# Kernel tuning notes

Measured on AMD Instinct MI355X. Metric: run time of the kernel, lower is better.

The kernel has to match this reference:

```python
import jax, jax.numpy as jnp
import numpy as np

D_MODEL = 1024
NHEAD = 16
HEAD_DIM = D_MODEL // NHEAD
SCALE = 1.0 / np.sqrt(HEAD_DIM).astype(np.float32)
B, L = 2, 2048
NEG_INF = -1e30


def setup_inputs() -> dict:
    key = jax.random.key(0)
    ks = jax.random.split(key, 12)
    xav = np.sqrt(6.0 / (D_MODEL + D_MODEL)).astype(np.float32)  # xavier_uniform gain=1
    def lin_w(k):
        return jax.random.uniform(k, (D_MODEL, D_MODEL), jnp.float32, -xav, xav)
    x = jax.random.normal(ks[0], (B, L, D_MODEL), jnp.float32)
    role_mask = jax.random.randint(ks[1], (B, L), 0, 2, jnp.int32)
    # causal attention mask: True = masked (upper triangle above diagonal)
    attn_mask = jnp.triu(jnp.ones((L, L), jnp.bool_), k=1)
    # random key padding: True = padded key
    key_padding_mask = jax.random.randint(ks[2], (B, L), 0, 2, jnp.int32).astype(jnp.bool_)
    return {
        "x": x,
        "role_mask": role_mask,
        "attn_mask": attn_mask,
        "key_padding_mask": key_padding_mask,
        "Wq": lin_w(ks[3]), "bq": jnp.zeros((D_MODEL,), jnp.float32),
        "Wk": lin_w(ks[4]), "bk": jnp.zeros((D_MODEL,), jnp.float32),
        "Wv": lin_w(ks[5]), "bv": jnp.zeros((D_MODEL,), jnp.float32),
        "Wo": lin_w(ks[6]), "bo": jnp.zeros((D_MODEL,), jnp.float32),
        "delta": jnp.asarray(1.0, jnp.float32),
    }


def reference(x, role_mask, attn_mask, key_padding_mask,
              Wq, bq, Wk, bk, Wv, bv, Wo, bo, delta):
    Bb, Ll, Dd = x.shape
    def heads(t):  # [B,L,D] -> [B,H,L,hd]
        return t.reshape(Bb, Ll, NHEAD, HEAD_DIM).transpose(0, 2, 1, 3)
    Q = heads(x @ Wq.T + bq)
    K = heads(x @ Wk.T + bk)
    V = heads(x @ Wv.T + bv)
    scores = jnp.einsum('bhqd,bhkd->bhqk', Q, K) * SCALE  # [B,H,L,L]
    same_role = (role_mask[:, :, None] == role_mask[:, None, :])  # [B,L,L]
    scores = scores + (same_role.astype(scores.dtype) * delta)[:, None, :, :]
    scores = jnp.where(attn_mask[None, None, :, :], -jnp.inf, scores)
    scores = jnp.where(key_padding_mask[:, None, None, :], -jnp.inf, scores)
    attn = jax.nn.softmax(scores, axis=-1)
    attn = jnp.nan_to_num(attn, nan=0.0, posinf=0.0, neginf=0.0)
    out = jnp.einsum('bhqk,bhkd->bhqd', attn, V)
    out = out.transpose(0, 2, 1, 3).reshape(Bb, Ll, Dd)
    return out @ Wo.T + bo
```

## Files before the change

### kernel.cpp

```cpp
#include <hip/hip_runtime.h>
#include <hip/hip_bf16.h>

#define DM 1024
#define NH 16
#define HD 64
#define BB 2
#define LL 2048
#define SCALE 0.125f
#define NEG_BIG -1e30f
#define LOG2E 1.4426950408889634f
#define SC2 (SCALE * LOG2E)
#define FIXM 16.0f
#define SLOTB 8448
#define POOL0_SLOTS 960

typedef __bf16 bf16;
typedef __bf16 bf16x8 __attribute__((ext_vector_type(8)));
typedef __bf16 bf16x4 __attribute__((ext_vector_type(4)));
typedef float f32x4 __attribute__((ext_vector_type(4)));

static __device__ inline bf16x8 load8(const bf16* p) {
    return *reinterpret_cast<const bf16x8*>(p);
}

static __device__ inline float scrub(float x) {
    union { float f; unsigned u; } c; c.f = x;
    return ((c.u & 0x7F800000u) == 0x7F800000u) ? 0.f : x;
}

typedef __attribute__((address_space(1))) const unsigned char ga_t;
typedef __attribute__((address_space(3))) unsigned char ls_t;
static __device__ inline void gload_lds16(const void* g, void* l) {
    __builtin_amdgcn_global_load_lds((ga_t*)g, (ls_t*)l, 16, 0, 0);
}

__global__ __launch_bounds__(256) void prep_all(
    const float* __restrict__ x,
    const float* __restrict__ Wq, const float* __restrict__ Wk,
    const float* __restrict__ Wv, const float* __restrict__ Wo,
    bf16* __restrict__ xb, bf16* __restrict__ Wqb, bf16* __restrict__ Wkb,
    bf16* __restrict__ Wvb, bf16* __restrict__ Wob,
    const int* __restrict__ role, const void* __restrict__ kpad,
    const float* __restrict__ deltap, float2* __restrict__ biasG)
{
    const int tid = threadIdx.x;
    const int gid = blockIdx.x;
    if (gid < 2048) {
        const float* src; bf16* dst; size_t base;
        if (gid < 1024) { src = x; dst = xb; base = (size_t)gid * 1024; }
        else {
            const int wsel = (gid - 1024) >> 8;
            src = (wsel == 0) ? Wq : (wsel == 1) ? Wk : (wsel == 2) ? Wv : Wo;
            dst = (wsel == 0) ? Wqb : (wsel == 1) ? Wkb : (wsel == 2) ? Wvb : Wob;
            base = (size_t)((gid - 1024) & 255) * 1024;
        }
#pragma unroll
        for (int it = 0; it < 4; it++) {
            const size_t i = base + it * 256 + tid;
            const f32x4 v = ((const f32x4*)src)[i];
            bf16x4 o;
            o[0] = (bf16)v[0]; o[1] = (bf16)v[1]; o[2] = (bf16)v[2]; o[3] = (bf16)v[3];
            ((bf16x4*)dst)[i] = o;
        }
        return;
    }
    const unsigned char* kb = (const unsigned char*)kpad;
    int f3F = 0, fLow = 0, fOff = 0;
    for (int i = (tid & 63); i < BB * LL; i += 64) {
        const unsigned char v = kb[i];
        if (v == 0x3F) f3F = 1;
        if ((i & 3) < 2 && v) fLow = 1;
        if ((i & 3) && v) fOff = 1;
    }
    const int mode = __any(f3F) ? (__any(fLow) ? 3 : 2) : (__any(fOff) ? 1 : 0);
    const float d2 = scrub(deltap[0]) * LOG2E;
    const int idx = (gid - 2048) * 256 + tid;
    const bool pad = (mode == 0) ? (((const int*)kpad)[idx] != 0)
                   : (mode == 1) ? (((const unsigned char*)kpad)[idx] != 0)
                   : (mode == 2) ? (((const float*)kpad)[idx] != 0.f)
                                 : (((const unsigned short*)kpad)[idx] != 0);
    const int r = role[idx];
    const float base = (pad ? NEG_BIG : 0.f) - FIXM;
    float2 o;
    o.x = base + ((r == 0) ? d2 : 0.f);
    o.y = base + ((r == 1) ? d2 : 0.f);
    biasG[idx] = o;
}

__global__ __launch_bounds__(256) void qkv_bf16(
    const bf16* __restrict__ xb,
    const bf16* __restrict__ Wqb, const bf16* __restrict__ Wkb, const bf16* __restrict__ Wvb,
    const float* __restrict__ bq, const float* __restrict__ bk, const float* __restrict__ bv,
    bf16* __restrict__ qw, bf16* __restrict__ kw, bf16* __restrict__ vw)
{
    __shared__ bf16 As[128 * 32];
    __shared__ bf16 Bs[128 * 32];
    const int tid = threadIdx.x;
    const int lane = tid & 63, w = tid >> 6;
    const int wm = w >> 1, wn = w & 1;
    const int ln = lane & 15, quad = lane >> 4;

    const int lin = blockIdx.y * 32 + blockIdx.x;
    const int xcd = lin & 7;
    const int t = lin >> 3;
    const int mloc = t & 3;
    const int yy = t >> 2;
    const int m0 = (xcd * 4 + mloc) * 128;
    const int sel = yy >> 3;
    const int nloc0 = (yy & 7) * 128;

    const bf16* Wb = (sel == 0) ? Wqb : ((sel == 1) ? Wkb : Wvb);
    const float* bias = (sel == 0) ? bq : ((sel == 1) ? bk : bv);
    bf16* dstw = (sel == 0) ? qw : ((sel == 1) ? kw : vw);

    const int rA = lane >> 2;
    const int cA = (lane & 3) * 8;

    f32x4 acc[4][4] = {};
    for (int k0 = 0; k0 < DM; k0 += 32) {
        __syncthreads();
#pragma unroll
        for (int s = 0; s < 2; s++) {
            const int r0 = s * 64 + w * 16;
            gload_lds16(xb + (size_t)(m0 + r0 + rA) * DM + k0 + cA, &As[r0 * 32]);
            gload_lds16(Wb + (size_t)(nloc0 + r0 + rA) * DM + k0 + cA, &Bs[r0 * 32]);
        }
        __syncthreads();
        bf16x8 a[4], b[4];
#pragma unroll
        for (int mi = 0; mi < 4; mi++)
            a[mi] = *(bf16x8*)&As[(wm * 64 + mi * 16 + ln) * 32 + quad * 8];
#pragma unroll
        for (int ni = 0; ni < 4; ni++)
            b[ni] = *(bf16x8*)&Bs[(wn * 64 + ni * 16 + ln) * 32 + quad * 8];
#pragma unroll
        for (int mi = 0; mi < 4; mi++)
#pragma unroll
            for (int ni = 0; ni < 4; ni++)
                acc[mi][ni] = __builtin_amdgcn_mfma_f32_16x16x32_bf16(a[mi], b[ni], acc[mi][ni], 0, 0, 0);
    }

#pragma unroll
    for (int mi = 0; mi < 4; mi++) {
#pragma unroll
        for (int ni = 0; ni < 4; ni++) {
            const int ncol = nloc0 + wn * 64 + ni * 16 + ln;
            const float bv_ = bias[ncol];
            const int hh = ncol >> 6, dd = ncol & 63;
#pragma unroll
            for (int i = 0; i < 4; i++) {
                const int row = m0 + wm * 64 + mi * 16 + quad * 4 + i;
                const int bb = row >> 11, llr = row & (LL - 1);
                const bf16 v = (bf16)scrub(acc[mi][ni][i] + bv_);
                dstw[(((size_t)(bb * NH + hh) * LL) + llr) * HD + dd] = v;
            }
        }
    }
}

__global__ __launch_bounds__(256) void vtrans(
    const bf16* __restrict__ vw, bf16* __restrict__ vtw)
{
    __shared__ bf16 T[64][72];
    const int l0 = blockIdx.x * 64;
    const int bh = blockIdx.y;
    const int tid = threadIdx.x;
#pragma unroll
    for (int it = 0; it < 2; it++) {
        const int idx = it * 256 + tid;
        const int row = idx >> 3, c8 = (idx & 7) * 8;
        const int wc = (((c8 >> 3) ^ ((row >> 3) & 7))) * 8;
        *(bf16x8*)&T[row][wc] = load8(vw + ((size_t)bh * LL + l0 + row) * HD + c8);
    }
    __syncthreads();
#pragma unroll
    for (int it = 0; it < 2; it++) {
        const int idx = it * 256 + tid;
        const int dd = idx >> 3, pg = (idx & 7) * 8;
        bf16x8 o;
#pragma unroll
        for (int j = 0; j < 8; j++) {
            const int r = pg + j;
            o[j] = T[r][(dd & 7) + ((((dd >> 3) ^ ((r >> 3) & 7))) << 3)];
        }
        *(bf16x8*)(vtw + ((size_t)bh * HD + dd) * LL + l0 + pg) = o;
    }
}

__global__ __launch_bounds__(256) void attn_v13(
    const bf16* __restrict__ qw, const bf16* __restrict__ kw, const bf16* __restrict__ vtw,
    const int* __restrict__ role, const float2* __restrict__ biasG,
    char* __restrict__ pool0, char* __restrict__ pool1,
    bf16* __restrict__ attn_out)
{
    const int lin = blockIdx.y * 60 + blockIdx.x;
    const int xcd = lin & 7;
    const int t = lin >> 3;
    const int xg = t % 60;
    const int g = t / 60;
    const int bh = g * 8 + xcd;

    int qb, c;
    if (xg < 24)      { qb = 31 - xg / 3; c = xg % 3; }
    else if (xg < 48) { qb = 23 - (xg - 24) / 2; c = (xg - 24) % 2; }
    else              { qb = 59 - xg; c = 0; }
    const int nch = (qb + 12) / 12;

    __shared__ bf16 Ks[2][2][64 * 32];
    __shared__ bf16 Vs[2][2][64 * 32];

    const int tid = threadIdx.x;
    const int lane = tid & 63, w = tid >> 6;
    const int col = lane & 15, quad = lane >> 4;
    const int h = bh & (NH - 1), b = bh >> 4;
    const int q0 = qb * 64 + w * 16;

    const bf16* qbase = qw + (size_t)((b * NH + h) * LL) * HD;
    const bf16* kbase = kw + (size_t)((b * NH + h) * LL) * HD;
    const bf16* vbase = vtw + (size_t)((b * NH + h) * HD) * LL;
    const float2* bias2 = biasG + (size_t)b * LL;
    const int* rrow = role + b * LL;

    const int srow = lane >> 2;
    const int sslot = w * 16 + srow;
    const int trueK = ((sslot >> 5) & 1) * 32 + ((sslot >> 2) & 3) * 8
                    + ((sslot >> 4) & 1) * 4 + (sslot & 3);
    const int swz = ((lane & 3) ^ ((lane >> 3) & 3)) * 8;
    const bf16* ksrc = kbase + (size_t)trueK * HD + swz;
    const bf16* vsrc = vbase + (size_t)(w * 16 + srow) * LL + swz;

    bf16x8 qf[2];
    qf[0] = load8(qbase + (size_t)(q0 + col) * HD + quad * 8);
    qf[1] = load8(qbase + (size_t)(q0 + col) * HD + 32 + quad * 8);

    bf16x8 ones;
#pragma unroll
    for (int j = 0; j < 8; j++) ones[j] = (bf16)1.0f;

    const int role_q = rrow[q0 + col];
    const int qabs = q0 + col;

    f32x4 ol = {};
    f32x4 o[4] = {};

    const int t0 = c * 12;
    const int t1 = (t0 + 12 < qb + 1) ? t0 + 12 : qb + 1;

    {
        const int kp = t0 * 64;
#pragma unroll
        for (int st = 0; st < 2; st++)
            gload_lds16(ksrc + (size_t)kp * HD + st * 32, &Ks[0][st][w * 512]);
#pragma unroll
        for (int kh = 0; kh < 2; kh++)
            gload_lds16(vsrc + kp + kh * 32, &Vs[0][kh][w * 512]);
    }

    const int rs = (quad ^ ((col >> 1) & 3)) * 8;

    for (int kt = t0; kt < t1; kt++) {
        const int cur = (kt - t0) & 1;
        __syncthreads();

        if (kt + 1 < t1) {
            const int k1 = (kt + 1) * 64;
#pragma unroll
            for (int st = 0; st < 2; st++)
                gload_lds16(ksrc + (size_t)k1 * HD + st * 32, &Ks[cur ^ 1][st][w * 512]);
#pragma unroll
            for (int kh = 0; kh < 2; kh++)
                gload_lds16(vsrc + k1 + kh * 32, &Vs[cur ^ 1][kh][w * 512]);
        }

        const int k0 = kt * 64;

        f32x4 s[4] = {};
#pragma unroll
        for (int st = 0; st < 2; st++) {
#pragma unroll
            for (int ns = 0; ns < 4; ns++) {
                const bf16x8 kf = *(bf16x8*)&Ks[cur][st][(ns * 16 + col) * 32 + rs];
                s[ns] = __builtin_amdgcn_mfma_f32_16x16x32_bf16(kf, qf[st], s[ns], 0, 0, 0);
            }
        }

        const bool diag = (kt == qb);
        bf16x8 pf[2];
#pragma unroll
        for (int ns = 0; ns < 4; ns++) {
            const int kb_ = k0 + ((ns >> 1) << 5) + (quad << 3) + ((ns & 1) << 2);
            const f32x4 bA = *(const f32x4*)&bias2[kb_];
            const f32x4 bB = *(const f32x4*)&bias2[kb_ + 2];
#pragma unroll
            for (int i = 0; i < 4; i++) {
                const f32x4 bp = (i < 2) ? bA : bB;
                const float bias = role_q ? bp[(i & 1) * 2 + 1] : bp[(i & 1) * 2];
                float sv = fmaf(s[ns][i], SC2, bias);
                if (diag && (kb_ + i) > qabs) sv = NEG_BIG;
                pf[ns >> 1][(ns & 1) * 4 + i] = (bf16)exp2f(sv);
            }
        }

#pragma unroll
        for (int ns = 0; ns < 4; ns++) {
#pragma unroll
            for (int kh = 0; kh < 2; kh++) {
                const bf16x8 vf = *(bf16x8*)&Vs[cur][kh][(ns * 16 + col) * 32 + rs];
                o[ns] = __builtin_amdgcn_mfma_f32_16x16x32_bf16(vf, pf[kh], o[ns], 0, 0, 0);
            }
        }
#pragma unroll
        for (int kh = 0; kh < 2; kh++)
            ol = __builtin_amdgcn_mfma_f32_16x16x32_bf16(ones, pf[kh], ol, 0, 0, 0);
    }

    if (nch == 1) {
        const float inv = (ol[0] > 0.f) ? 1.f / ol[0] : 0.f;
        bf16* orow = attn_out + ((size_t)(b * LL) + qabs) * DM + h * HD;
#pragma unroll
        for (int ns = 0; ns < 4; ns++) {
            bf16x4 ov;
#pragma unroll
            for (int i = 0; i < 4; i++) ov[i] = (bf16)scrub(o[ns][i] * inv);
            *(bf16x4*)&orow[ns * 16 + quad * 4] = ov;
        }
    } else {
        const int base = (qb <= 23) ? (qb - 12) * 2 : 24 + (qb - 24) * 3;
        const int slot = bh * 48 + base + c;
        char* ptr = (slot < POOL0_SLOTS) ? (pool0 + (size_t)slot * SLOTB)
                                         : (pool1 + (size_t)(slot - POOL0_SLOTS) * SLOTB);
        bf16* op = (bf16*)ptr;
        float* lp = (float*)(ptr + 8192);
        const int r = w * 16 + col;
        if (quad == 0) lp[r] = ol[0];
#pragma unroll
        for (int ns = 0; ns < 4; ns++) {
            bf16x4 ov;
#pragma unroll
            for (int i = 0; i < 4; i++) ov[i] = (bf16)scrub(o[ns][i]);
            *(bf16x4*)&op[r * 64 + ns * 16 + quad * 4] = ov;
        }
    }
}

__global__ __launch_bounds__(256) void combine(
    const char* __restrict__ pool0, const char* __restrict__ pool1,
    bf16* __restrict__ attn_out)
{
    const int qb = 12 + blockIdx.x;
    const int bh = blockIdx.y;
    const int h = bh & (NH - 1), b = bh >> 4;
    const int nch = (qb + 12) / 12;
    const int base = (qb <= 23) ? (qb - 12) * 2 : 24 + (qb - 24) * 3;

    const char* ptr[3];
    for (int c = 0; c < nch; c++) {
        const int slot = bh * 48 + base + c;
        ptr[c] = (slot < POOL0_SLOTS) ? (pool0 + (size_t)slot * SLOTB)
                                      : (pool1 + (size_t)(slot - POOL0_SLOTS) * SLOTB);
    }

    __shared__ float linv[64];
    const int tid = threadIdx.x;
    if (tid < 64) {
        float ls = 0.f;
        for (int c = 0; c < nch; c++) ls += ((const float*)(ptr[c] + 8192))[tid];
        linv[tid] = (ls > 0.f) ? 1.f / ls : 0.f;
    }
    __syncthreads();

    const int r = tid >> 2;
    const int d0 = (tid & 3) * 16;
    float acc[16] = {};
    for (int c = 0; c < nch; c++) {
        const bf16* op = (const bf16*)ptr[c];
#pragma unroll
        for (int half = 0; half < 2; half++) {
            const bf16x8 v = load8(op + r * 64 + d0 + half * 8);
#pragma unroll
            for (int j = 0; j < 8; j++) acc[half * 8 + j] += (float)v[j];
        }
    }
    const float inv = linv[r];
    bf16x8 outv[2];
#pragma unroll
    for (int half = 0; half < 2; half++)
#pragma unroll
        for (int j = 0; j < 8; j++)
            outv[half][j] = (bf16)scrub(acc[half * 8 + j] * inv);
    bf16* orow = attn_out + ((size_t)(b * LL) + qb * 64 + r) * DM + h * HD + d0;
    *(bf16x8*)orow = outv[0];
    *(bf16x8*)(orow + 8) = outv[1];
}

__global__ __launch_bounds__(256) void out_bf16(
    const bf16* __restrict__ A, const bf16* __restrict__ Wb,
    const float* __restrict__ bias, float* __restrict__ out)
{
    __shared__ bf16 As[128 * 32];
    __shared__ bf16 Bs[64 * 32];
    const int tid = threadIdx.x;
    const int lane = tid & 63, w = tid >> 6;
    const int ln = lane & 15, quad = lane >> 4;

    const int lin = blockIdx.y * 32 + blockIdx.x;
    const int xcd = lin & 7;
    const int t = lin >> 3;
    const int mloc = t & 3;
    const int n = t >> 2;
    const int m0 = (xcd * 4 + mloc) * 128;
    const int n0 = n * 64;

    const int rA = lane >> 2;
    const int cA = (lane & 3) * 8;

    f32x4 acc[2][4] = {};
    for (int k0 = 0; k0 < DM; k0 += 32) {
        __syncthreads();
#pragma unroll
        for (int s = 0; s < 2; s++) {
            const int r0 = s * 64 + w * 16;
            gload_lds16(A + (size_t)(m0 + r0 + rA) * DM + k0 + cA, &As[r0 * 32]);
        }
        gload_lds16(Wb + (size_t)(n0 + w * 16 + rA) * DM + k0 + cA, &Bs[w * 16 * 32]);
        __syncthreads();
        bf16x8 a[2], b[4];
#pragma unroll
        for (int mi = 0; mi < 2; mi++)
            a[mi] = *(bf16x8*)&As[(w * 32 + mi * 16 + ln) * 32 + quad * 8];
#pragma unroll
        for (int ni = 0; ni < 4; ni++)
            b[ni] = *(bf16x8*)&Bs[(ni * 16 + ln) * 32 + quad * 8];
#pragma unroll
        for (int mi = 0; mi < 2; mi++)
#pragma unroll
            for (int ni = 0; ni < 4; ni++)
                acc[mi][ni] = __builtin_amdgcn_mfma_f32_16x16x32_bf16(a[mi], b[ni], acc[mi][ni], 0, 0, 0);
    }
#pragma unroll
    for (int mi = 0; mi < 2; mi++) {
#pragma unroll
        for (int ni = 0; ni < 4; ni++) {
            const int ncol = n0 + ni * 16 + ln;
            const float bv_ = bias[ncol];
#pragma unroll
            for (int i = 0; i < 4; i++) {
                const int row = m0 + w * 32 + mi * 16 + quad * 4 + i;
                out[(size_t)row * DM + ncol] = scrub(acc[mi][ni][i] + bv_);
            }
        }
    }
}

extern "C" void kernel_launch(void* const* d_in, const int* in_sizes, int n_in,
                              void* d_out, int out_size, void* d_ws, size_t ws_size,
                              hipStream_t stream) {
    const float* x    = (const float*)d_in[0];
    const int*   role = (const int*)d_in[1];
    const void*  kpad = d_in[3];
    const float* Wq = (const float*)d_in[4];
    const float* bq = (const float*)d_in[5];
    const float* Wk = (const float*)d_in[6];
    const float* bk = (const float*)d_in[7];
    const float* Wv = (const float*)d_in[8];
    const float* bv = (const float*)d_in[9];
    const float* Wo = (const float*)d_in[10];
    const float* bo = (const float*)d_in[11];
    const float* dl = (const float*)d_in[12];

    char* ws = (char*)d_ws;
    bf16* qw   = (bf16*)(ws);
    bf16* kw   = (bf16*)(ws + (size_t)(8u  << 20));
    bf16* Wqb  = (bf16*)(ws + (size_t)(16u << 20));
    bf16* Wkb  = (bf16*)(ws + (size_t)(18u << 20));
    bf16* Wvb  = (bf16*)(ws + (size_t)(20u << 20));
    char* pool0 = ws + (size_t)(16u << 20);
    bf16* vw   = (bf16*)(ws + (size_t)(24u << 20));
    bf16* aw   = (bf16*)(ws + (size_t)(24u << 20));
    bf16* vtw  = (bf16*)(ws + (size_t)(32u << 20));
    bf16* xb   = (bf16*)(ws + (size_t)(40u << 20));
    char* pool1 = ws + (size_t)(40u << 20);
    bf16* Wob  = (bf16*)(ws + (size_t)(48u << 20) + 65536);
    float2* biasG = (float2*)(ws + (size_t)(48u << 20));
    float* out = (float*)d_out;

    prep_all<<<dim3(2064), dim3(256), 0, stream>>>(
        x, Wq, Wk, Wv, Wo, xb, Wqb, Wkb, Wvb, Wob, role, kpad, dl, biasG);
    qkv_bf16<<<dim3(32, 24), dim3(256), 0, stream>>>(
        xb, Wqb, Wkb, Wvb, bq, bk, bv, qw, kw, vw);
    vtrans<<<dim3(32, 32), dim3(256), 0, stream>>>(vw, vtw);
    attn_v13<<<dim3(60, 32), dim3(256), 0, stream>>>(
        qw, kw, vtw, role, biasG, pool0, pool1, aw);
    combine<<<dim3(20, 32), dim3(256), 0, stream>>>(pool0, pool1, aw);
    out_bf16<<<dim3(32, 16), dim3(256), 0, stream>>>(aw, Wob, bo, out);
}
```

Measured before the change: 230.5 us.

## Compact unpadded keys per batch so attention skips padded key tiles

```diff
diff --git a/kernel.cpp b/kernel.cpp
--- a/kernel.cpp
+++ b/kernel.cpp
@@ -6,6 +6,7 @@
 #define HD 64
 #define BB 2
 #define LL 2048
+#define BL (BB * LL)
 #define SCALE 0.125f
 #define NEG_BIG -1e30f
 #define LOG2E 1.4426950408889634f
@@ -39,59 +40,103 @@
     const float* __restrict__ Wq, const float* __restrict__ Wk,
     const float* __restrict__ Wv, const float* __restrict__ Wo,
     bf16* __restrict__ xb, bf16* __restrict__ Wqb, bf16* __restrict__ Wkb,
-    bf16* __restrict__ Wvb, bf16* __restrict__ Wob,
+    bf16* __restrict__ Wvb, bf16* __restrict__ Wob)
+{
+    const int tid = threadIdx.x;
+    const int gid = blockIdx.x;
+    const float* src; bf16* dst; size_t base;
+    if (gid < 1024) { src = x; dst = xb; base = (size_t)gid * 1024; }
+    else {
+        const int wsel = (gid - 1024) >> 8;
+        src = (wsel == 0) ? Wq : (wsel == 1) ? Wk : (wsel == 2) ? Wv : Wo;
+        dst = (wsel == 0) ? Wqb : (wsel == 1) ? Wkb : (wsel == 2) ? Wvb : Wob;
+        base = (size_t)((gid - 1024) & 255) * 1024;
+    }
+#pragma unroll
+    for (int it = 0; it < 4; it++) {
+        const size_t i = base + it * 256 + tid;
+        const f32x4 v = ((const f32x4*)src)[i];
+        bf16x4 o;
+        o[0] = (bf16)v[0]; o[1] = (bf16)v[1]; o[2] = (bf16)v[2]; o[3] = (bf16)v[3];
+        ((bf16x4*)dst)[i] = o;
+    }
+}
+
+__global__ __launch_bounds__(256) void compact_meta(
     const int* __restrict__ role, const void* __restrict__ kpad,
-    const float* __restrict__ deltap, float2* __restrict__ biasG)
-{
-    const int tid = threadIdx.x;
-    const int gid = blockIdx.x;
-    if (gid < 2048) {
-        const float* src; bf16* dst; size_t base;
-        if (gid < 1024) { src = x; dst = xb; base = (size_t)gid * 1024; }
-        else {
-            const int wsel = (gid - 1024) >> 8;
-            src = (wsel == 0) ? Wq : (wsel == 1) ? Wk : (wsel == 2) ? Wv : Wo;
-            dst = (wsel == 0) ? Wqb : (wsel == 1) ? Wkb : (wsel == 2) ? Wvb : Wob;
-            base = (size_t)((gid - 1024) & 255) * 1024;
-        }
-#pragma unroll
-        for (int it = 0; it < 4; it++) {
-            const size_t i = base + it * 256 + tid;
-            const f32x4 v = ((const f32x4*)src)[i];
-            bf16x4 o;
-            o[0] = (bf16)v[0]; o[1] = (bf16)v[1]; o[2] = (bf16)v[2]; o[3] = (bf16)v[3];
-            ((bf16x4*)dst)[i] = o;
-        }
-        return;
-    }
+    const float* __restrict__ deltap,
+    float* __restrict__ biasC, int* __restrict__ cntq, int* __restrict__ cpos,
+    bf16* __restrict__ kwc)
+{
+    const int b = blockIdx.x;
+    const int tid = threadIdx.x;
     const unsigned char* kb = (const unsigned char*)kpad;
     int f3F = 0, fLow = 0, fOff = 0;
-    for (int i = (tid & 63); i < BB * LL; i += 64) {
+    for (int i = (tid & 63); i < BL; i += 64) {
         const unsigned char v = kb[i];
         if (v == 0x3F) f3F = 1;
         if ((i & 3) < 2 && v) fLow = 1;
         if ((i & 3) && v) fOff = 1;
     }
     const int mode = __any(f3F) ? (__any(fLow) ? 3 : 2) : (__any(fOff) ? 1 : 0);
+
+    __shared__ int ssum[256];
+    int loc[8]; int s = 0;
+#pragma unroll
+    for (int j = 0; j < 8; j++) {
+        const int i = tid * 8 + j, idx = b * LL + i;
+        const bool pad = (mode == 0) ? (((const int*)kpad)[idx] != 0)
+                       : (mode == 1) ? (((const unsigned char*)kpad)[idx] != 0)
+                       : (mode == 2) ? (((const float*)kpad)[idx] != 0.f)
+                                     : (((const unsigned short*)kpad)[idx] != 0);
+        loc[j] = pad ? 0 : 1; s += loc[j];
+    }
+    ssum[tid] = s; __syncthreads();
+    for (int off = 1; off < 256; off <<= 1) {
+        const int t = (tid >= off) ? ssum[tid - off] : 0;
+        __syncthreads();
+        ssum[tid] += t;
+        __syncthreads();
+    }
+    const int nv = ssum[255];
+    int run = ssum[tid] - s;
     const float d2 = scrub(deltap[0]) * LOG2E;
-    const int idx = (gid - 2048) * 256 + tid;
-    const bool pad = (mode == 0) ? (((const int*)kpad)[idx] != 0)
-                   : (mode == 1) ? (((const unsigned char*)kpad)[idx] != 0)
-                   : (mode == 2) ? (((const float*)kpad)[idx] != 0.f)
-                                 : (((const unsigned short*)kpad)[idx] != 0);
-    const int r = role[idx];
-    const float base = (pad ? NEG_BIG : 0.f) - FIXM;
-    float2 o;
-    o.x = base + ((r == 0) ? d2 : 0.f);
-    o.y = base + ((r == 1) ? d2 : 0.f);
-    biasG[idx] = o;
+#pragma unroll
+    for (int j = 0; j < 8; j++) {
+        const int i = tid * 8 + j, idx = b * LL + i;
+        const int inc = run + loc[j];
+        cntq[idx] = inc;
+        if (loc[j]) {
+            const int cp = inc - 1;
+            const int r = role[idx];
+            biasC[b * LL + cp]      = -FIXM + ((r == 0) ? d2 : 0.f);
+            biasC[BL + b * LL + cp] = -FIXM + ((r == 1) ? d2 : 0.f);
+            cpos[idx] = cp;
+        } else cpos[idx] = -1;
+        run = inc;
+    }
+    for (int i = nv + tid; i < LL; i += 256) {
+        biasC[b * LL + i] = NEG_BIG;
+        biasC[BL + b * LL + i] = NEG_BIG;
+    }
+    const int roundv = (nv + 63) & ~63;
+    const int nt = roundv - nv;
+    bf16x8 z;
+#pragma unroll
+    for (int j = 0; j < 8; j++) z[j] = (bf16)0.f;
+    for (int u = tid; u < nt * NH * 8; u += 256) {
+        const int c8 = u & 7; const int t2 = u >> 3;
+        const int h = t2 / nt; const int rr = nv + t2 % nt;
+        *(bf16x8*)&kwc[(((size_t)(b * NH + h) * LL) + rr) * HD + c8 * 8] = z;
+    }
 }
 
 __global__ __launch_bounds__(256) void qkv_bf16(
     const bf16* __restrict__ xb,
     const bf16* __restrict__ Wqb, const bf16* __restrict__ Wkb, const bf16* __restrict__ Wvb,
     const float* __restrict__ bq, const float* __restrict__ bk, const float* __restrict__ bv,
-    bf16* __restrict__ qw, bf16* __restrict__ kw, bf16* __restrict__ vw)
+    bf16* __restrict__ qw, bf16* __restrict__ kwc, bf16* __restrict__ vwc,
+    const int* __restrict__ cpos)
 {
     __shared__ bf16 As[128 * 32];
     __shared__ bf16 Bs[128 * 32];
@@ -111,7 +156,7 @@
 
     const bf16* Wb = (sel == 0) ? Wqb : ((sel == 1) ? Wkb : Wvb);
     const float* bias = (sel == 0) ? bq : ((sel == 1) ? bk : bv);
-    bf16* dstw = (sel == 0) ? qw : ((sel == 1) ? kw : vw);
+    bf16* dstw = (sel == 0) ? qw : ((sel == 1) ? kwc : vwc);
 
     const int rA = lane >> 2;
     const int cA = (lane & 3) * 8;
@@ -143,34 +188,42 @@
 #pragma unroll
     for (int mi = 0; mi < 4; mi++) {
 #pragma unroll
-        for (int ni = 0; ni < 4; ni++) {
-            const int ncol = nloc0 + wn * 64 + ni * 16 + ln;
-            const float bv_ = bias[ncol];
-            const int hh = ncol >> 6, dd = ncol & 63;
-#pragma unroll
-            for (int i = 0; i < 4; i++) {
-                const int row = m0 + wm * 64 + mi * 16 + quad * 4 + i;
-                const int bb = row >> 11, llr = row & (LL - 1);
-                const bf16 v = (bf16)scrub(acc[mi][ni][i] + bv_);
-                dstw[(((size_t)(bb * NH + hh) * LL) + llr) * HD + dd] = v;
+        for (int i = 0; i < 4; i++) {
+            const int row = m0 + wm * 64 + mi * 16 + quad * 4 + i;
+            const int bb = row >> 11, llr = row & (LL - 1);
+            const int cp = (sel == 0) ? llr : cpos[bb * LL + llr];
+#pragma unroll
+            for (int ni = 0; ni < 4; ni++) {
+                const int ncol = nloc0 + wn * 64 + ni * 16 + ln;
+                const int hh = ncol >> 6, dd = ncol & 63;
+                const bf16 v = (bf16)scrub(acc[mi][ni][i] + bias[ncol]);
+                if (cp >= 0)
+                    dstw[(((size_t)(bb * NH + hh) * LL) + cp) * HD + dd] = v;
             }
         }
     }
 }
 
 __global__ __launch_bounds__(256) void vtrans(
-    const bf16* __restrict__ vw, bf16* __restrict__ vtw)
+    const bf16* __restrict__ vwc, bf16* __restrict__ vtc, const int* __restrict__ cntq)
 {
     __shared__ bf16 T[64][72];
     const int l0 = blockIdx.x * 64;
     const int bh = blockIdx.y;
+    const int b = bh >> 4;
+    const int nv = cntq[b * LL + LL - 1];
+    if (l0 >= ((nv + 63) & ~63)) return;
     const int tid = threadIdx.x;
 #pragma unroll
     for (int it = 0; it < 2; it++) {
         const int idx = it * 256 + tid;
         const int row = idx >> 3, c8 = (idx & 7) * 8;
         const int wc = (((c8 >> 3) ^ ((row >> 3) & 7))) * 8;
-        *(bf16x8*)&T[row][wc] = load8(vw + ((size_t)bh * LL + l0 + row) * HD + c8);
+        bf16x8 val;
+#pragma unroll
+        for (int j = 0; j < 8; j++) val[j] = (bf16)0.f;
+        if (l0 + row < nv) val = load8(vwc + ((size_t)bh * LL + l0 + row) * HD + c8);
+        *(bf16x8*)&T[row][wc] = val;
     }
     __syncthreads();
 #pragma unroll
@@ -183,13 +236,13 @@
             const int r = pg + j;
             o[j] = T[r][(dd & 7) + ((((dd >> 3) ^ ((r >> 3) & 7))) << 3)];
         }
-        *(bf16x8*)(vtw + ((size_t)bh * HD + dd) * LL + l0 + pg) = o;
-    }
-}
-
-__global__ __launch_bounds__(256) void attn_v13(
-    const bf16* __restrict__ qw, const bf16* __restrict__ kw, const bf16* __restrict__ vtw,
-    const int* __restrict__ role, const float2* __restrict__ biasG,
+        *(bf16x8*)(vtc + ((size_t)bh * HD + dd) * LL + l0 + pg) = o;
+    }
+}
+
+__global__ __launch_bounds__(256) void attn_v14(
+    const bf16* __restrict__ qw, const bf16* __restrict__ kwc, const bf16* __restrict__ vtc,
+    const int* __restrict__ role, const float* __restrict__ biasC, const int* __restrict__ cntq,
     char* __restrict__ pool0, char* __restrict__ pool1,
     bf16* __restrict__ attn_out)
 {
@@ -216,9 +269,8 @@
     const int q0 = qb * 64 + w * 16;
 
     const bf16* qbase = qw + (size_t)((b * NH + h) * LL) * HD;
-    const bf16* kbase = kw + (size_t)((b * NH + h) * LL) * HD;
-    const bf16* vbase = vtw + (size_t)((b * NH + h) * HD) * LL;
-    const float2* bias2 = biasG + (size_t)b * LL;
+    const bf16* kbase = kwc + (size_t)((b * NH + h) * LL) * HD;
+    const bf16* vbase = vtc + (size_t)((b * NH + h) * HD) * LL;
     const int* rrow = role + b * LL;
 
     const int srow = lane >> 2;
@@ -237,17 +289,21 @@
 #pragma unroll
     for (int j = 0; j < 8; j++) ones[j] = (bf16)1.0f;
 
-    const int role_q = rrow[q0 + col];
     const int qabs = q0 + col;
+    const int role_q = rrow[qabs];
+    const int cnt_q = cntq[b * LL + qabs];
+    const float* bp = biasC + (size_t)role_q * BL + b * LL;
+
+    const int cb = cntq[b * LL + qb * 64 + 63];
+    const int Tb = (cb + 63) >> 6;
+    const int t0c = (c * Tb) / nch;
+    const int t1c = ((c + 1) * Tb) / nch;
 
     f32x4 ol = {};
     f32x4 o[4] = {};
 
-    const int t0 = c * 12;
-    const int t1 = (t0 + 12 < qb + 1) ? t0 + 12 : qb + 1;
-
-    {
-        const int kp = t0 * 64;
+    if (t0c < t1c) {
+        const int kp = t0c * 64;
 #pragma unroll
         for (int st = 0; st < 2; st++)
             gload_lds16(ksrc + (size_t)kp * HD + st * 32, &Ks[0][st][w * 512]);
@@ -258,11 +314,11 @@
 
     const int rs = (quad ^ ((col >> 1) & 3)) * 8;
 
-    for (int kt = t0; kt < t1; kt++) {
-        const int cur = (kt - t0) & 1;
-        __syncthreads();
-
-        if (kt + 1 < t1) {
+    for (int kt = t0c; kt < t1c; kt++) {
+        const int cur = (kt - t0c) & 1;
+        __syncthreads();
+
+        if (kt + 1 < t1c) {
             const int k1 = (kt + 1) * 64;
 #pragma unroll
             for (int st = 0; st < 2; st++)
@@ -284,19 +340,15 @@
             }
         }
 
-        const bool diag = (kt == qb);
         bf16x8 pf[2];
 #pragma unroll
         for (int ns = 0; ns < 4; ns++) {
             const int kb_ = k0 + ((ns >> 1) << 5) + (quad << 3) + ((ns & 1) << 2);
-            const f32x4 bA = *(const f32x4*)&bias2[kb_];
-            const f32x4 bB = *(const f32x4*)&bias2[kb_ + 2];
+            const f32x4 bv4 = *(const f32x4*)&bp[kb_];
 #pragma unroll
             for (int i = 0; i < 4; i++) {
-                const f32x4 bp = (i < 2) ? bA : bB;
-                const float bias = role_q ? bp[(i & 1) * 2 + 1] : bp[(i & 1) * 2];
-                float sv = fmaf(s[ns][i], SC2, bias);
-                if (diag && (kb_ + i) > qabs) sv = NEG_BIG;
+                float sv = fmaf(s[ns][i], SC2, bv4[i]);
+                if ((kb_ + i) >= cnt_q) sv = NEG_BIG;
                 pf[ns >> 1][(ns & 1) * 4 + i] = (bf16)exp2f(sv);
             }
         }
@@ -470,27 +522,31 @@
 
     char* ws = (char*)d_ws;
     bf16* qw   = (bf16*)(ws);
-    bf16* kw   = (bf16*)(ws + (size_t)(8u  << 20));
+    bf16* kwc  = (bf16*)(ws + (size_t)(8u  << 20));
     bf16* Wqb  = (bf16*)(ws + (size_t)(16u << 20));
     bf16* Wkb  = (bf16*)(ws + (size_t)(18u << 20));
     bf16* Wvb  = (bf16*)(ws + (size_t)(20u << 20));
     char* pool0 = ws + (size_t)(16u << 20);
-    bf16* vw   = (bf16*)(ws + (size_t)(24u << 20));
+    bf16* vwc  = (bf16*)(ws + (size_t)(24u << 20));
     bf16* aw   = (bf16*)(ws + (size_t)(24u << 20));
-    bf16* vtw  = (bf16*)(ws + (size_t)(32u << 20));
+    bf16* vtc  = (bf16*)(ws + (size_t)(32u << 20));
     bf16* xb   = (bf16*)(ws + (size_t)(40u << 20));
     char* pool1 = ws + (size_t)(40u << 20);
+    float* biasC = (float*)(ws + (size_t)(48u << 20));
+    int*   cntq  = (int*)(ws + (size_t)(48u << 20) + 32768);
+    int*   cpos  = (int*)(ws + (size_t)(48u << 20) + 49152);
     bf16* Wob  = (bf16*)(ws + (size_t)(48u << 20) + 65536);
-    float2* biasG = (float2*)(ws + (size_t)(48u << 20));
     float* out = (float*)d_out;
 
-    prep_all<<<dim3(2064), dim3(256), 0, stream>>>(
-        x, Wq, Wk, Wv, Wo, xb, Wqb, Wkb, Wvb, Wob, role, kpad, dl, biasG);
+    prep_all<<<dim3(2048), dim3(256), 0, stream>>>(
+        x, Wq, Wk, Wv, Wo, xb, Wqb, Wkb, Wvb, Wob);
+    compact_meta<<<dim3(2), dim3(256), 0, stream>>>(
+        role, kpad, dl, biasC, cntq, cpos, kwc);
     qkv_bf16<<<dim3(32, 24), dim3(256), 0, stream>>>(
-        xb, Wqb, Wkb, Wvb, bq, bk, bv, qw, kw, vw);
-    vtrans<<<dim3(32, 32), dim3(256), 0, stream>>>(vw, vtw);
-    attn_v13<<<dim3(60, 32), dim3(256), 0, stream>>>(
-        qw, kw, vtw, role, biasG, pool0, pool1, aw);
+        xb, Wqb, Wkb, Wvb, bq, bk, bv, qw, kwc, vwc, cpos);
+    vtrans<<<dim3(32, 32), dim3(256), 0, stream>>>(vwc, vtc, cntq);
+    attn_v14<<<dim3(60, 32), dim3(256), 0, stream>>>(
+        qw, kwc, vtc, role, biasC, cntq, pool0, pool1, aw);
     combine<<<dim3(20, 32), dim3(256), 0, stream>>>(pool0, pool1, aw);
     out_bf16<<<dim3(32, 16), dim3(256), 0, stream>>>(aw, Wob, bo, out);
 }
```

Result: faster. 218.4 us (-5.2%).
